# Kernel optimization log

Measured on AMD Instinct MI355X. Metric: run time of the kernel, lower is better.

## Reference

```python
import jax, jax.numpy as jnp
import numpy as np

D = 256          # embed_dim
NH = 4           # num_heads
NE = 16          # num_hyperedges
TC = 512         # text_channels
WIN = 64         # window size
EPS = 1e-5


def setup_inputs() -> dict:
    key = jax.random.key(0)
    ks = jax.random.split(key, 20)
    s = 0.02
    return {
        "feature_map": jax.random.normal(ks[0], (8, 256, 64, 64), jnp.float32),
        "text_features": jax.random.normal(ks[1], (8, 64, TC), jnp.float32),
        # qkv_gen: Conv2d(256->256,1x1), GELU, Conv2d(256->768,3x3,pad1), GroupNorm(4,768)
        "conv1_w": jax.random.normal(ks[2], (D, 256, 1, 1), jnp.float32) * s,
        "conv1_b": jnp.zeros((D,), jnp.float32),
        "conv2_w": jax.random.normal(ks[3], (3 * D, D, 3, 3), jnp.float32) * s,
        "conv2_b": jnp.zeros((3 * D,), jnp.float32),
        "gn_w": jnp.ones((3 * D,), jnp.float32),
        "gn_b": jnp.zeros((3 * D,), jnp.float32),
        # shared nn.MultiheadAttention params
        "in_proj_w": jax.random.normal(ks[4], (3 * D, D), jnp.float32) * s,
        "in_proj_b": jnp.zeros((3 * D,), jnp.float32),
        "out_proj_w": jax.random.normal(ks[5], (D, D), jnp.float32) * s,
        "out_proj_b": jnp.zeros((D,), jnp.float32),
        # text_adapter Linear(512->256)
        "txt_w": jax.random.normal(ks[6], (D, TC), jnp.float32) * s,
        "txt_b": jnp.zeros((D,), jnp.float32),
        # edge_predictor: Linear(512->256), GELU, Linear(256->16)
        "ep1_w": jax.random.normal(ks[7], (D, 2 * D), jnp.float32) * s,
        "ep1_b": jnp.zeros((D,), jnp.float32),
        "ep2_w": jax.random.normal(ks[8], (NE, D), jnp.float32) * s,
        "ep2_b": jnp.zeros((NE,), jnp.float32),
    }


def _gelu(x):
    return jax.nn.gelu(x, approximate=False)  # torch default is exact erf GELU


def _conv(x, w, b, pad):
    y = jax.lax.conv_general_dilated(x, w, (1, 1), [(pad, pad), (pad, pad)],
                                     dimension_numbers=("NCHW", "OIHW", "NCHW"))
    return y + b[None, :, None, None]


def _group_norm(x, w, b, groups=4):
    B, C, H, W = x.shape
    xg = x.reshape(B, groups, C // groups, H, W)
    mu = xg.mean(axis=(2, 3, 4), keepdims=True)
    var = xg.var(axis=(2, 3, 4), keepdims=True)
    xg = (xg - mu) * jax.lax.rsqrt(var + EPS)
    return xg.reshape(B, C, H, W) * w[None, :, None, None] + b[None, :, None, None]


def _mha(q, k, v, in_w, in_b, out_w, out_b):
    # torch nn.MultiheadAttention (batch_first), same-dim q/k/v
    Wq, Wk, Wv = in_w[:D], in_w[D:2 * D], in_w[2 * D:]
    bq, bk, bv = in_b[:D], in_b[D:2 * D], in_b[2 * D:]
    dh = D // NH

    def split(x, W, bias):
        y = x @ W.T + bias                      # [B,L,D]
        Bv, L, _ = y.shape
        return y.reshape(Bv, L, NH, dh).transpose(0, 2, 1, 3)  # [B,H,L,dh]

    qh, kh, vh = split(q, Wq, bq), split(k, Wk, bk), split(v, Wv, bv)
    scores = jnp.einsum("bhqd,bhkd->bhqk", qh, kh) / jnp.sqrt(jnp.float32(dh))
    attn = jax.nn.softmax(scores, axis=-1)
    o = jnp.einsum("bhqk,bhkd->bhqd", attn, vh)
    Bv, _, Lq, _ = o.shape
    o = o.transpose(0, 2, 1, 3).reshape(Bv, Lq, D)
    return o @ out_w.T + out_b


def reference(feature_map, text_features, conv1_w, conv1_b, conv2_w, conv2_b,
              gn_w, gn_b, in_proj_w, in_proj_b, out_proj_w, out_proj_b,
              txt_w, txt_b, ep1_w, ep1_b, ep2_w, ep2_b):
    B, C, H, W = feature_map.shape
    N = H * W
    # qkv_gen
    x = _gelu(_conv(feature_map, conv1_w, conv1_b, 0))
    qkv = _group_norm(_conv(x, conv2_w, conv2_b, 1), gn_w, gn_b)
    q, k, v = jnp.split(qkv, 3, axis=1)                    # each [B,D,H,W]
    to_seq = lambda t: t.reshape(B, D, N).transpose(0, 2, 1)  # [B,N,D]
    q_seq, k_seq, v_seq = to_seq(q), to_seq(k), to_seq(v)

    # text_adapter: Linear then AdaptiveAvgPool1d(4) over sequence (L=64 -> 4 bins of 16)
    t = text_features @ txt_w.T + txt_b                    # [B,L,D]
    L = t.shape[1]
    text_feat = t.reshape(B, 4, L // 4, D).mean(axis=2)    # [B,4,D]

    # hierarchical attention
    nw = N // WIN
    q_win = q_seq.reshape(B * nw, WIN, D)
    k_win = k_seq.reshape(B * nw, WIN, D)
    v_win = v_seq.reshape(B * nw, WIN, D)
    local = _mha(q_win, k_win, v_win, in_proj_w, in_proj_b, out_proj_w, out_proj_b)
    local = local.reshape(B, nw, WIN, D)
    global_q = local.mean(axis=2)                          # [B,nw,D]
    glob = _mha(global_q, text_feat, text_feat, in_proj_w, in_proj_b, out_proj_w, out_proj_b)
    glob = jnp.broadcast_to(glob[:, :, None, :], (B, nw, WIN, D))

    combined = jnp.concatenate([local.reshape(B, N, D), glob.reshape(B, N, D)], axis=-1)
    h = _gelu(combined @ ep1_w.T + ep1_b)
    return jax.nn.sigmoid(h @ ep2_w.T + ep2_b)             # [B,N,16]
```

## Files before the change

kernel.cpp:

```cpp
#include <hip/hip_runtime.h>

#define DEV __device__ __forceinline__

typedef __attribute__((ext_vector_type(8))) short bfx8;
typedef __attribute__((ext_vector_type(4))) float fx4;

typedef __attribute__((address_space(3))) unsigned int as3_u32;
typedef const __attribute__((address_space(1))) unsigned int as1_u32c;

DEV void gl_lds16(const void* g, const void* l) {
  __builtin_amdgcn_global_load_lds((as1_u32c*)(unsigned long long)g,
                                   (as3_u32*)(unsigned long long)l, 16, 0, 0);
}

DEV short f2bf(float f) {
  unsigned u = __float_as_uint(f);
  u += 0x7fffu + ((u >> 16) & 1u);
  return (short)(u >> 16);
}
DEV float bf2f(short s) {
  return __uint_as_float(((unsigned)(unsigned short)s) << 16);
}
DEV float gelu_f(float x) { return 0.5f * x * (1.0f + erff(x * 0.70710678118654752f)); }

#define MFMA16(acc, a, b) (acc) = __builtin_amdgcn_mfma_f32_16x16x32_bf16((a), (b), (acc), 0, 0, 0)

struct PrepArgs {
  const float *w1, *inw, *ow, *tw, *e1w, *e2w, *txt, *w2, *e1b, *ob, *tb, *inb;
  short *W1bf, *Wqkv, *Wo, *Wtxt, *Wep1, *Wep2, *W2t, *Wcomb;
  float *ebc, *khv, *vhv;
};

__global__ __launch_bounds__(256) void prep(PrepArgs a) {
  __shared__ char shmem[34816];
  const int bid = (int)blockIdx.x;
  const int t = threadIdx.x;
  if (bid < 290) {
    const float* src; short* dst; int st;
    if (bid < 32)       { src = a.w1;  dst = a.W1bf; st = 0; }
    else if (bid < 128) { src = a.inw; dst = a.Wqkv; st = 32; }
    else if (bid < 160) { src = a.ow;  dst = a.Wo;   st = 128; }
    else if (bid < 224) { src = a.tw;  dst = a.Wtxt; st = 160; }
    else if (bid < 288) { src = a.e1w; dst = a.Wep1; st = 224; }
    else                { src = a.e2w; dst = a.Wep2; st = 288; }
    long i = ((long)(bid - st) * 256 + t) * 8;
    bfx8 o;
    #pragma unroll
    for (int j = 0; j < 8; ++j) o[j] = f2bf(src[i + j]);
    *(bfx8*)(dst + i) = o;
  } else if (bid < 1058) {
    int oc = (bid - 290) * 256 + t;
    const float* s = a.w2 + (long)oc * 9;
    float v[9];
    #pragma unroll
    for (int j = 0; j < 9; ++j) v[j] = s[j];
    #pragma unroll
    for (int tap = 0; tap < 9; ++tap)
      a.W2t[(long)tap * (768 * 256) + oc] = f2bf(v[tap]);
  } else if (bid < 1122) {
    int n = (bid - 1058) * 4 + (t >> 6);
    int lane = t & 63;
    float s = 0.0f;
    #pragma unroll
    for (int i = 0; i < 4; ++i) {
      int c = lane + 64 * i;
      s += a.ob[c] * a.e1w[(long)n * 512 + c];
    }
    #pragma unroll
    for (int off = 1; off < 64; off <<= 1) s += __shfl_xor(s, off);
    if (lane == 0) a.ebc[n] = a.e1b[n] + s;
  } else if (bid < 1130) {
    float* tmean = (float*)shmem;
    float* tfb = (float*)(shmem + 8192);
    const int b = bid - 1122;
    {
      int key = t >> 6, d0 = (t & 63) * 8;
      float s[8] = {};
      const float* src = a.txt + ((long)(b * 64 + key * 16)) * 512 + d0;
      for (int i = 0; i < 16; ++i) {
        fx4 v0 = *(const fx4*)(src + (long)i * 512);
        fx4 v1 = *(const fx4*)(src + (long)i * 512 + 4);
        #pragma unroll
        for (int j = 0; j < 4; ++j) { s[j] += v0[j]; s[4 + j] += v1[j]; }
      }
      #pragma unroll
      for (int j = 0; j < 8; ++j) tmean[key * 512 + d0 + j] = s[j] * (1.0f / 16.0f);
    }
    __syncthreads();
    {
      int n = t;
      float a0 = 0, a1 = 0, a2 = 0, a3 = 0;
      const float* wr = a.tw + (long)n * 512;
      for (int d = 0; d < 512; d += 4) {
        fx4 w = *(const fx4*)(wr + d);
        #pragma unroll
        for (int j = 0; j < 4; ++j) {
          float wf = w[j];
          a0 += tmean[0 * 512 + d + j] * wf;
          a1 += tmean[1 * 512 + d + j] * wf;
          a2 += tmean[2 * 512 + d + j] * wf;
          a3 += tmean[3 * 512 + d + j] * wf;
        }
      }
      float bias = a.tb[n];
      tfb[0 * 256 + n] = a0 + bias; tfb[1 * 256 + n] = a1 + bias;
      tfb[2 * 256 + n] = a2 + bias; tfb[3 * 256 + n] = a3 + bias;
    }
    __syncthreads();
    {
      int n = t;
      const float* wk = a.inw + (long)(256 + n) * 256;
      const float* wvp = a.inw + (long)(512 + n) * 256;
      float k0=0,k1=0,k2=0,k3=0,v0=0,v1=0,v2=0,v3=0;
      for (int d = 0; d < 256; d += 4) {
        fx4 wkv = *(const fx4*)(wk + d);
        fx4 wvv = *(const fx4*)(wvp + d);
        #pragma unroll
        for (int j = 0; j < 4; ++j) {
          float f0 = tfb[0*256+d+j], f1 = tfb[1*256+d+j], f2 = tfb[2*256+d+j], f3 = tfb[3*256+d+j];
          float kw = wkv[j], vw = wvv[j];
          k0 += f0*kw; k1 += f1*kw; k2 += f2*kw; k3 += f3*kw;
          v0 += f0*vw; v1 += f1*vw; v2 += f2*vw; v3 += f3*vw;
        }
      }
      float bk = a.inb[256+n], bv = a.inb[512+n];
      a.khv[(b*4+0)*256+n]=k0+bk; a.khv[(b*4+1)*256+n]=k1+bk;
      a.khv[(b*4+2)*256+n]=k2+bk; a.khv[(b*4+3)*256+n]=k3+bk;
      a.vhv[(b*4+0)*256+n]=v0+bv; a.vhv[(b*4+1)*256+n]=v1+bv;
      a.vhv[(b*4+2)*256+n]=v2+bv; a.vhv[(b*4+3)*256+n]=v3+bv;
    }
  } else {
    short* Bt = (short*)shmem;
    const int idx = bid - 1130;
    const int bx = idx & 3, by = idx >> 2;
    const int lane = t & 63, w = t >> 6;
    const int lg = lane >> 4, li = lane & 15;
    const int m0 = by * 64, n0 = bx * 64;
    for (int id2 = t; id2 < 64 * 256; id2 += 256) {
      int c = id2 >> 6, d = id2 & 63;
      Bt[d * 264 + c] = f2bf(a.ow[(long)c * 256 + n0 + d]);
    }
    __syncthreads();
    fx4 acc[4] = {};
    const float* aR = a.e1w + (long)(m0 + w * 16 + li) * 512 + lg * 8;
    for (int kc = 0; kc < 256; kc += 32) {
      fx4 lo = *(const fx4*)(aR + kc);
      fx4 hi = *(const fx4*)(aR + kc + 4);
      bfx8 av;
      av[0] = f2bf(lo[0]); av[1] = f2bf(lo[1]); av[2] = f2bf(lo[2]); av[3] = f2bf(lo[3]);
      av[4] = f2bf(hi[0]); av[5] = f2bf(hi[1]); av[6] = f2bf(hi[2]); av[7] = f2bf(hi[3]);
      #pragma unroll
      for (int ni = 0; ni < 4; ++ni) {
        bfx8 bv = *(const bfx8*)(&Bt[(ni * 16 + li) * 264 + kc + lg * 8]);
        MFMA16(acc[ni], av, bv);
      }
    }
    #pragma unroll
    for (int ni = 0; ni < 4; ++ni)
      #pragma unroll
      for (int r = 0; r < 4; ++r)
        a.Wcomb[(long)(m0 + w * 16 + 4 * lg + r) * 256 + n0 + ni * 16 + li] = f2bf(acc[ni][r]);
  }
}

DEV int axc(int p, int c) { return p * 260 + (c ^ (((p >> 2) & 7) << 2)); }

__global__ __launch_bounds__(256) void tc1(const float* fm, const short* W1bf,
                                           const float* b1, short* xP) {
  __shared__ float Af[64 * 260];
  const int lane = threadIdx.x & 63, wv = threadIdx.x >> 6;
  const int lg = lane >> 4, li = lane & 15;
  const int y = blockIdx.x & 63, b = blockIdx.x >> 6;
  const int t = threadIdx.x;
  short* dstP = xP + ((long)b * 66 * 66 + (long)(y + 1) * 66 + 1) * 256;
  const bfx8 z8 = {0, 0, 0, 0, 0, 0, 0, 0};

  if (t < 64) {
    if (t < 32) *(bfx8*)(dstP - 256 + t * 8) = z8;
    else        *(bfx8*)(dstP + 64 * 256 + (t - 32) * 8) = z8;
  }
  if (y == 0) {
    short* top = xP + (long)b * 66 * 66 * 256;
    for (int i = t; i < 2112; i += 256) *(bfx8*)(top + i * 8) = z8;
  }
  if (y == 63) {
    short* bot = xP + ((long)b * 66 * 66 + 65 * 66) * 256;
    for (int i = t; i < 2112; i += 256) *(bfx8*)(bot + i * 8) = z8;
  }

  const float* src = fm + (long)b * 256 * 4096 + y * 64;
  #pragma unroll
  for (int i = 0; i < 16; ++i) {
    int chunk = i * 256 + t;
    int c = chunk >> 4;
    int q = chunk & 15;
    fx4 v = *(const fx4*)(src + (long)c * 4096 + q * 4);
    #pragma unroll
    for (int j = 0; j < 4; ++j) Af[axc(q * 4 + j, c)] = v[j];
  }
  __syncthreads();

  fx4 acc[4][4] = {};
  const short* Bb = W1bf + (long)(wv * 64 + li) * 256 + lg * 8;
  for (int c0 = 0; c0 < 256; c0 += 32) {
    bfx8 af[4], bfr[4];
    #pragma unroll
    for (int mi = 0; mi < 4; ++mi) {
      int p = mi * 16 + li;
      fx4 lo = *(const fx4*)(&Af[axc(p, c0 + lg * 8)]);
      fx4 hi = *(const fx4*)(&Af[axc(p, c0 + lg * 8 + 4)]);
      bfx8 tt;
      tt[0] = f2bf(lo[0]); tt[1] = f2bf(lo[1]); tt[2] = f2bf(lo[2]); tt[3] = f2bf(lo[3]);
      tt[4] = f2bf(hi[0]); tt[5] = f2bf(hi[1]); tt[6] = f2bf(hi[2]); tt[7] = f2bf(hi[3]);
      af[mi] = tt;
    }
    #pragma unroll
    for (int ni = 0; ni < 4; ++ni) bfr[ni] = *(const bfx8*)(Bb + ni * 16 * 256 + c0);
    #pragma unroll
    for (int mi = 0; mi < 4; ++mi)
      #pragma unroll
      for (int ni = 0; ni < 4; ++ni) MFMA16(acc[mi][ni], af[mi], bfr[ni]);
  }

  #pragma unroll
  for (int mi = 0; mi < 4; ++mi)
    #pragma unroll
    for (int ni = 0; ni < 4; ++ni) {
      int col = wv * 64 + ni * 16 + li;
      float bias = b1[col];
      #pragma unroll
      for (int r = 0; r < 4; ++r) {
        int x = mi * 16 + 4 * lg + r;
        dstP[(long)x * 256 + col] = f2bf(gelu_f(acc[mi][ni][r] + bias));
      }
    }
}

struct GemmP {
  const short* A; const short* B; void* O;
  const float* biasN; const float* biasM;
  long lda, ldb, ldo, sA, sB, sO;
  int M, N, K, outF32, act;
  int aShift;
  long sBN, sBM;
};

DEV void gemm_body64(const GemmP& g, int bx, int by, int bz) {
  __shared__ short As[2 * 128 * 32];
  __shared__ short Bs[2 * 128 * 32];
  const int lane = threadIdx.x & 63, wv = threadIdx.x >> 6;
  const int wm = wv >> 1, wn = wv & 1;
  const int lg = lane >> 4, li = lane & 15;
  const int m0 = by * 128, n0 = bx * 128, z = bz;
  const short* A = g.A + (long)z * g.sA + (long)(n0 >> 8) * g.aShift;
  const short* B = g.B + (long)z * g.sB;
  const int srow = wv * 16 + (lane >> 2);
  const int scol = (lane & 3) * 8;
  const short* pA0 = A + (long)(m0 + srow) * g.lda + scol;
  const short* pA1 = A + (long)(m0 + 64 + srow) * g.lda + scol;
  const short* pB0 = B + (long)(n0 + srow) * g.ldb + scol;
  const short* pB1 = B + (long)(n0 + 64 + srow) * g.ldb + scol;
  short* ldsA = As + wv * 512;
  short* ldsB = Bs + wv * 512;
  const short* aRd = As + (wm * 64 + li) * 32 + lg * 8;
  const short* bRd = Bs + (wn * 64 + li) * 32 + lg * 8;

  fx4 acc[4][4] = {};
  for (int kc = 0; kc < g.K; kc += 64) {
    gl_lds16(pA0 + kc, ldsA);
    gl_lds16(pA1 + kc, ldsA + 2048);
    gl_lds16(pA0 + kc + 32, ldsA + 4096);
    gl_lds16(pA1 + kc + 32, ldsA + 6144);
    gl_lds16(pB0 + kc, ldsB);
    gl_lds16(pB1 + kc, ldsB + 2048);
    gl_lds16(pB0 + kc + 32, ldsB + 4096);
    gl_lds16(pB1 + kc + 32, ldsB + 6144);
    __syncthreads();
    #pragma unroll
    for (int kk = 0; kk < 2; ++kk) {
      bfx8 af[4], bf[4];
      #pragma unroll
      for (int mi = 0; mi < 4; ++mi) af[mi] = *(const bfx8*)(aRd + kk * 4096 + mi * 16 * 32);
      #pragma unroll
      for (int ni = 0; ni < 4; ++ni) bf[ni] = *(const bfx8*)(bRd + kk * 4096 + ni * 16 * 32);
      #pragma unroll
      for (int mi = 0; mi < 4; ++mi)
        #pragma unroll
        for (int ni = 0; ni < 4; ++ni)
          MFMA16(acc[mi][ni], af[mi], bf[ni]);
    }
    __syncthreads();
  }

  #pragma unroll
  for (int mi = 0; mi < 4; ++mi)
    #pragma unroll
    for (int ni = 0; ni < 4; ++ni) {
      int col = n0 + wn * 64 + ni * 16 + li;
      int rowb = m0 + wm * 64 + mi * 16 + 4 * lg;
      float bn = g.biasN ? g.biasN[(long)z * g.sBN + col] : 0.0f;
      #pragma unroll
      for (int r = 0; r < 4; ++r) {
        int row = rowb + r;
        float v = acc[mi][ni][r] + bn;
        if (g.biasM) v += g.biasM[(long)z * g.sBM + row];
        if (g.act == 1) v = gelu_f(v);
        long oidx = (long)z * g.sO + (long)row * g.ldo + col;
        if (g.outF32) ((float*)g.O)[oidx] = v;
        else ((short*)g.O)[oidx] = f2bf(v);
      }
    }
}

__global__ __launch_bounds__(256) void projk(GemmP gq, GemmP gv) {
  int bid = (int)blockIdx.x;
  int id = (bid & 7) * 192 + (bid >> 3);
  if (id < 1024) {
    int z = id >> 7, r = id & 127;
    gemm_body64(gq, r & 3, r >> 2, z);
  } else {
    int j = id - 1024;
    int z = j >> 6, r = j & 63;
    gemm_body64(gv, r & 31, r >> 5, z);
  }
}

__global__ __launch_bounds__(256) void conv2g(const short* xP, const short* W2t,
                                              const float* b2, short* qkv, float* stats) {
  __shared__ short As[2 * 128 * 32];
  __shared__ short Bs[2 * 128 * 32];
  __shared__ float red[4][4];
  const int lane = threadIdx.x & 63, wv = threadIdx.x >> 6;
  const int wm = wv >> 1, wn = wv & 1;
  const int lg = lane >> 4, li = lane & 15;
  const int w = ((int)blockIdx.x & 7) * 192 + ((int)blockIdx.x >> 3);
  const int n0 = (w % 6) * 128;
  const int by = w / 6;
  const int b = by >> 5, ypair = by & 31;
  const short* xPb = xP + (long)b * 66 * 66 * 256;

  const int srow = wv * 16 + (lane >> 2);
  const int scol = (lane & 3) * 8;
  long baseA[2], baseB[2];
  #pragma unroll
  for (int j = 0; j < 2; ++j) {
    int r = j * 64 + srow;
    int yy = 2 * ypair + (r >> 6);
    int x = r & 63;
    baseA[j] = ((long)yy * 66 + x) * 256 + scol;
    baseB[j] = (long)(n0 + r) * 256 + scol;
  }
  short* ldsA = As + wv * 512;
  short* ldsB = Bs + wv * 512;
  const short* aRd = As + (wm * 64 + li) * 32 + lg * 8;
  const short* bRd = Bs + (wn * 64 + li) * 32 + lg * 8;

  fx4 acc[4][4] = {};
  for (int ks = 0; ks < 36; ++ks) {
    int tap = ks >> 2;
    int c0 = (ks & 3) * 64;
    int dy = tap / 3, dx = tap - dy * 3;
    long aoff = (long)(dy * 66 + dx) * 256 + c0;
    long boff = (long)tap * (768 * 256) + c0;
    gl_lds16(xPb + baseA[0] + aoff, ldsA);
    gl_lds16(xPb + baseA[1] + aoff, ldsA + 2048);
    gl_lds16(xPb + baseA[0] + aoff + 32, ldsA + 4096);
    gl_lds16(xPb + baseA[1] + aoff + 32, ldsA + 6144);
    gl_lds16(W2t + baseB[0] + boff, ldsB);
    gl_lds16(W2t + baseB[1] + boff, ldsB + 2048);
    gl_lds16(W2t + baseB[0] + boff + 32, ldsB + 4096);
    gl_lds16(W2t + baseB[1] + boff + 32, ldsB + 6144);
    __syncthreads();
    #pragma unroll
    for (int kk = 0; kk < 2; ++kk) {
      bfx8 af[4], bf[4];
      #pragma unroll
      for (int mi = 0; mi < 4; ++mi) af[mi] = *(const bfx8*)(aRd + kk * 4096 + mi * 16 * 32);
      #pragma unroll
      for (int ni = 0; ni < 4; ++ni) bf[ni] = *(const bfx8*)(bRd + kk * 4096 + ni * 16 * 32);
      #pragma unroll
      for (int mi = 0; mi < 4; ++mi)
        #pragma unroll
        for (int ni = 0; ni < 4; ++ni)
          MFMA16(acc[mi][ni], af[mi], bf[ni]);
    }
    __syncthreads();
  }

  const int g0 = n0 / 192;
  const int bnd = (g0 + 1) * 192;
  float sA = 0.0f, s2A = 0.0f, sB = 0.0f, s2B = 0.0f;
  const long prow0 = (long)b * 4096 + (long)ypair * 128 + wm * 64 + 4 * lg;
  #pragma unroll
  for (int ni = 0; ni < 4; ++ni) {
    int col = n0 + wn * 64 + ni * 16 + li;
    float bias = b2[col];
    bool inA = (col < bnd);
    #pragma unroll
    for (int mi = 0; mi < 4; ++mi) {
      long rb = prow0 + mi * 16;
      #pragma unroll
      for (int r = 0; r < 4; ++r) {
        float v = acc[mi][ni][r] + bias;
        if (inA) { sA += v; s2A += v * v; } else { sB += v; s2B += v * v; }
        qkv[(rb + r) * 768 + col] = f2bf(v);
      }
    }
  }
  #pragma unroll
  for (int off = 1; off < 64; off <<= 1) {
    sA += __shfl_xor(sA, off);  s2A += __shfl_xor(s2A, off);
    sB += __shfl_xor(sB, off);  s2B += __shfl_xor(s2B, off);
  }
  if (lane == 0) { red[wv][0] = sA; red[wv][1] = s2A; red[wv][2] = sB; red[wv][3] = s2B; }
  __syncthreads();
  if (threadIdx.x == 0) {
    float a1 = red[0][0] + red[1][0] + red[2][0] + red[3][0];
    float a2 = red[0][1] + red[1][1] + red[2][1] + red[3][1];
    atomicAdd(&stats[(b * 4 + g0) * 2], a1);
    atomicAdd(&stats[(b * 4 + g0) * 2 + 1], a2);
    if (bnd < n0 + 128) {
      float b1s = red[0][2] + red[1][2] + red[2][2] + red[3][2];
      float b2s = red[0][3] + red[1][3] + red[2][3] + red[3][3];
      atomicAdd(&stats[(b * 4 + g0 + 1) * 2], b1s);
      atomicAdd(&stats[(b * 4 + g0 + 1) * 2 + 1], b2s);
    }
  }
}

__global__ __launch_bounds__(256) void gn_fold(const float* stats, const float* gnw, const float* gnb,
                                               const float* inw, const float* inb,
                                               short* Wf, float* bfold) {
  const int lane = threadIdx.x & 63, wv = threadIdx.x >> 6;
  const int row = blockIdx.x * 4 + wv;
  const int b = row / 768, j = row - b * 768;
  const int cb = (j >> 8) << 8;
  const float nrm = 1.0f / (192.0f * 4096.0f);
  float part = 0.0f;
  #pragma unroll
  for (int i = 0; i < 4; ++i) {
    int c = lane + 64 * i;
    int cg = cb + c;
    int grp = cg / 192;
    float s1 = stats[(b * 4 + grp) * 2];
    float s2 = stats[(b * 4 + grp) * 2 + 1];
    float mu = s1 * nrm;
    float var = s2 * nrm - mu * mu;
    float rs = rsqrtf(var + 1e-5f);
    float s = rs * gnw[cg];
    float t = gnb[cg] - mu * s;
    float wv_ = inw[(long)j * 256 + c];
    Wf[(long)row * 256 + c] = f2bf(wv_ * s);
    part += t * wv_;
  }
  #pragma unroll
  for (int off = 1; off < 64; off <<= 1) part += __shfl_xor(part, off);
  if (lane == 0) bfold[row] = inb[j] + part;
}

__global__ __launch_bounds__(256) void attn_local(const short* qk, const short* vhT,
                                                  short* oat, short* oatm) {
  __shared__ short Pl[4 * 64 * 72];
  const int lane = threadIdx.x & 63, h = threadIdx.x >> 6;
  const int lg = lane >> 4, li = lane & 15;
  const int bw = blockIdx.x;
  const int b = bw >> 6, wY = bw & 63;
  const long p0 = (long)bw * 64;

  bfx8 qf[4][2], kf[4][2];
  #pragma unroll
  for (int mi = 0; mi < 4; ++mi)
    #pragma unroll
    for (int ks = 0; ks < 2; ++ks) {
      qf[mi][ks] = *(const bfx8*)(qk + (p0 + 16 * mi + li) * 512 + h * 64 + 32 * ks + 8 * lg);
      kf[mi][ks] = *(const bfx8*)(qk + (p0 + 16 * mi + li) * 512 + 256 + h * 64 + 32 * ks + 8 * lg);
    }
  fx4 s[4][4] = {};
  #pragma unroll
  for (int mi = 0; mi < 4; ++mi)
    #pragma unroll
    for (int ni = 0; ni < 4; ++ni) {
      MFMA16(s[mi][ni], qf[mi][0], kf[ni][0]);
      MFMA16(s[mi][ni], qf[mi][1], kf[ni][1]);
    }
  #pragma unroll
  for (int mi = 0; mi < 4; ++mi)
    #pragma unroll
    for (int ni = 0; ni < 4; ++ni) s[mi][ni] *= 0.125f;

  #pragma unroll
  for (int mi = 0; mi < 4; ++mi)
    #pragma unroll
    for (int r = 0; r < 4; ++r) {
      float mx = fmaxf(fmaxf(s[mi][0][r], s[mi][1][r]), fmaxf(s[mi][2][r], s[mi][3][r]));
      for (int off = 1; off < 16; off <<= 1) mx = fmaxf(mx, __shfl_xor(mx, off));
      float e[4];
      float sum = 0.0f;
      #pragma unroll
      for (int ni = 0; ni < 4; ++ni) { e[ni] = expf(s[mi][ni][r] - mx); sum += e[ni]; }
      for (int off = 1; off < 16; off <<= 1) sum += __shfl_xor(sum, off);
      float inv = 1.0f / sum;
      int row = h * 64 + 16 * mi + 4 * lg + r;
      #pragma unroll
      for (int ni = 0; ni < 4; ++ni) Pl[row * 72 + 16 * ni + li] = f2bf(e[ni] * inv);
    }
  __syncthreads();

  fx4 o[4][4] = {};
  #pragma unroll
  for (int ks = 0; ks < 2; ++ks) {
    bfx8 pf[4], vf[4];
    #pragma unroll
    for (int mi = 0; mi < 4; ++mi)
      pf[mi] = *(const bfx8*)(&Pl[(h * 64 + 16 * mi + li) * 72 + 32 * ks + 8 * lg]);
    #pragma unroll
    for (int ni = 0; ni < 4; ++ni)
      vf[ni] = *(const bfx8*)(vhT + ((long)(b * 256 + h * 64 + 16 * ni + li)) * 4096 + wY * 64 + 32 * ks + 8 * lg);
    #pragma unroll
    for (int mi = 0; mi < 4; ++mi)
      #pragma unroll
      for (int ni = 0; ni < 4; ++ni) MFMA16(o[mi][ni], pf[mi], vf[ni]);
  }
  #pragma unroll
  for (int mi = 0; mi < 4; ++mi)
    #pragma unroll
    for (int ni = 0; ni < 4; ++ni)
      #pragma unroll
      for (int r = 0; r < 4; ++r)
        oat[(p0 + 16 * mi + 4 * lg + r) * 256 + h * 64 + 16 * ni + li] = f2bf(o[mi][ni][r]);

  #pragma unroll
  for (int ni = 0; ni < 4; ++ni) {
    float s2 = 0.0f;
    #pragma unroll
    for (int mi = 0; mi < 4; ++mi)
      #pragma unroll
      for (int r = 0; r < 4; ++r) s2 += o[mi][ni][r];
    s2 += __shfl_xor(s2, 16);
    s2 += __shfl_xor(s2, 32);
    if (lg == 0)
      oatm[(long)bw * 256 + h * 64 + 16 * ni + li] = f2bf(s2 * (1.0f / 64.0f));
  }
}

#define GP 272

DEV void mm_stage(const short* srcA, const short* Bw, long ldb, const float* biasN,
                  short* dstL, float* dstG, int wv, int lg, int li) {
  fx4 acc[4][4] = {};
  const short* aRd = srcA + li * GP + lg * 8;
  const short* bR = Bw + (long)(wv * 64 + li) * ldb + lg * 8;
  for (int kc = 0; kc < 256; kc += 32) {
    bfx8 af[4], bf[4];
    #pragma unroll
    for (int mi = 0; mi < 4; ++mi) af[mi] = *(const bfx8*)(aRd + mi * 16 * GP + kc);
    #pragma unroll
    for (int ni = 0; ni < 4; ++ni) bf[ni] = *(const bfx8*)(bR + (long)ni * 16 * ldb + kc);
    #pragma unroll
    for (int mi = 0; mi < 4; ++mi)
      #pragma unroll
      for (int ni = 0; ni < 4; ++ni) MFMA16(acc[mi][ni], af[mi], bf[ni]);
  }
  #pragma unroll
  for (int mi = 0; mi < 4; ++mi)
    #pragma unroll
    for (int ni = 0; ni < 4; ++ni) {
      int col = wv * 64 + ni * 16 + li;
      float bn = biasN[col];
      #pragma unroll
      for (int r = 0; r < 4; ++r) {
        int row = mi * 16 + 4 * lg + r;
        float v = acc[mi][ni][r] + bn;
        if (dstL) dstL[row * GP + col] = f2bf(v);
        else dstG[(long)row * 256 + col] = v;
      }
    }
}

__global__ __launch_bounds__(256) void globk2(
    const short* oatm, const float* khv, const float* vhv,
    const short* Wo, const short* Wqkv, const short* Wep1,
    const float* ob, const float* inb, const float* ebc,
    float* gcon) {
  __shared__ short bufA[64 * GP];
  __shared__ short bufB[64 * GP];
  __shared__ float kh_s[4][256];
  __shared__ float vh_s[4][256];
  const int t = threadIdx.x;
  const int lane = t & 63, wv = t >> 6;
  const int lg = lane >> 4, li = lane & 15;
  const int b = blockIdx.x;

  {
    #pragma unroll
    for (int i = 0; i < 8; ++i) {
      int chunk = i * 256 + t;
      int row = chunk >> 5, colc = (chunk & 31) * 8;
      *(bfx8*)(bufA + row * GP + colc) =
          *(const bfx8*)(oatm + ((long)(b * 64 + row)) * 256 + colc);
    }
    #pragma unroll
    for (int key = 0; key < 4; ++key) {
      kh_s[key][t] = khv[(long)(b * 4 + key) * 256 + t];
      vh_s[key][t] = vhv[(long)(b * 4 + key) * 256 + t];
    }
  }
  __syncthreads();
  mm_stage(bufA, Wo, 256, ob, bufB, nullptr, wv, lg, li);
  __syncthreads();
  mm_stage(bufB, Wqkv, 256, inb, bufA, nullptr, wv, lg, li);
  __syncthreads();
  {
    int p = t >> 2, h = t & 3;
    const short* qr = bufA + p * GP + h * 64;
    float sc[4];
    #pragma unroll
    for (int key = 0; key < 4; ++key) {
      float s = 0.0f;
      for (int d = 0; d < 64; d += 8) {
        bfx8 q8 = *(const bfx8*)(qr + d);
        #pragma unroll
        for (int j = 0; j < 8; ++j) s += bf2f(q8[j]) * kh_s[key][h * 64 + d + j];
      }
      sc[key] = s * 0.125f;
    }
    float mx = fmaxf(fmaxf(sc[0], sc[1]), fmaxf(sc[2], sc[3]));
    float e0 = expf(sc[0]-mx), e1 = expf(sc[1]-mx), e2 = expf(sc[2]-mx), e3 = expf(sc[3]-mx);
    float inv = 1.0f / (e0 + e1 + e2 + e3);
    e0 *= inv; e1 *= inv; e2 *= inv; e3 *= inv;
    short* orow = bufB + p * GP + h * 64;
    for (int d = 0; d < 64; ++d) {
      float o = e0*vh_s[0][h*64+d] + e1*vh_s[1][h*64+d] + e2*vh_s[2][h*64+d] + e3*vh_s[3][h*64+d];
      orow[d] = f2bf(o);
    }
  }
  __syncthreads();
  mm_stage(bufB, Wo, 256, ob, bufA, nullptr, wv, lg, li);
  __syncthreads();
  mm_stage(bufA, Wep1 + 256, 512, ebc, nullptr, gcon + (long)b * 64 * 256, wv, lg, li);
}

__global__ __launch_bounds__(256) void ep12(const short* oat, const short* Wcomb,
                                            const short* Wep2, const float* gcon,
                                            const float* e2b, float* out) {
  __shared__ short As[2 * 128 * 32];
  __shared__ short Bs[2 * 128 * 32];
  __shared__ short hl[128 * 140];
  const int lane = threadIdx.x & 63, wv = threadIdx.x >> 6;
  const int wm = wv >> 1, wn = wv & 1;
  const int lg = lane >> 4, li = lane & 15;
  const int m0 = (int)blockIdx.x * 128;
  const int srow = wv * 16 + (lane >> 2);
  const int scol = (lane & 3) * 8;
  const short* pA0 = oat + (long)(m0 + srow) * 256 + scol;
  const short* pA1 = oat + (long)(m0 + 64 + srow) * 256 + scol;
  short* ldsA = As + wv * 512;
  short* ldsB = Bs + wv * 512;
  const short* aRd = As + (wm * 64 + li) * 32 + lg * 8;
  const short* bRd = Bs + (wn * 64 + li) * 32 + lg * 8;

  fx4 eacc[2] = {};
  for (int half = 0; half < 2; ++half) {
    const short* B = Wcomb + (long)(half * 128) * 256;
    const short* pB0 = B + (long)srow * 256 + scol;
    const short* pB1 = B + (long)(64 + srow) * 256 + scol;
    fx4 acc[4][4] = {};
    for (int kc = 0; kc < 256; kc += 64) {
      gl_lds16(pA0 + kc, ldsA);
      gl_lds16(pA1 + kc, ldsA + 2048);
      gl_lds16(pA0 + kc + 32, ldsA + 4096);
      gl_lds16(pA1 + kc + 32, ldsA + 6144);
      gl_lds16(pB0 + kc, ldsB);
      gl_lds16(pB1 + kc, ldsB + 2048);
      gl_lds16(pB0 + kc + 32, ldsB + 4096);
      gl_lds16(pB1 + kc + 32, ldsB + 6144);
      __syncthreads();
      #pragma unroll
      for (int kk = 0; kk < 2; ++kk) {
        bfx8 af[4], bf[4];
        #pragma unroll
        for (int mi = 0; mi < 4; ++mi) af[mi] = *(const bfx8*)(aRd + kk * 4096 + mi * 16 * 32);
        #pragma unroll
        for (int ni = 0; ni < 4; ++ni) bf[ni] = *(const bfx8*)(bRd + kk * 4096 + ni * 16 * 32);
        #pragma unroll
        for (int mi = 0; mi < 4; ++mi)
          #pragma unroll
          for (int ni = 0; ni < 4; ++ni)
            MFMA16(acc[mi][ni], af[mi], bf[ni]);
      }
      __syncthreads();
    }
    #pragma unroll
    for (int mi = 0; mi < 4; ++mi)
      #pragma unroll
      for (int ni = 0; ni < 4; ++ni) {
        int coll = wn * 64 + ni * 16 + li;
        int colg = half * 128 + coll;
        #pragma unroll
        for (int r = 0; r < 4; ++r) {
          int rowl = wm * 64 + mi * 16 + 4 * lg + r;
          float v = acc[mi][ni][r] + gcon[(long)((m0 + rowl) >> 6) * 256 + colg];
          hl[rowl * 140 + coll] = f2bf(gelu_f(v));
        }
      }
    __syncthreads();
    #pragma unroll
    for (int kc = 0; kc < 128; kc += 32) {
      bfx8 bf2v = *(const bfx8*)(Wep2 + (long)li * 256 + half * 128 + kc + lg * 8);
      #pragma unroll
      for (int mi = 0; mi < 2; ++mi) {
        bfx8 af = *(const bfx8*)(hl + (wv * 32 + mi * 16 + li) * 140 + kc + lg * 8);
        MFMA16(eacc[mi], af, bf2v);
      }
    }
    __syncthreads();
  }
  #pragma unroll
  for (int mi = 0; mi < 2; ++mi)
    #pragma unroll
    for (int r = 0; r < 4; ++r) {
      int row = m0 + wv * 32 + mi * 16 + 4 * lg + r;
      out[(long)row * 16 + li] = 1.0f / (1.0f + expf(-(eacc[mi][r] + e2b[li])));
    }
}

extern "C" void kernel_launch(void* const* d_in, const int* in_sizes, int n_in,
                              void* d_out, int out_size, void* d_ws, size_t ws_size,
                              hipStream_t stream) {
  (void)in_sizes; (void)n_in; (void)out_size; (void)ws_size;
  const float* fm  = (const float*)d_in[0];
  const float* txt = (const float*)d_in[1];
  const float* w1  = (const float*)d_in[2];
  const float* b1  = (const float*)d_in[3];
  const float* w2  = (const float*)d_in[4];
  const float* b2  = (const float*)d_in[5];
  const float* gnw = (const float*)d_in[6];
  const float* gnb = (const float*)d_in[7];
  const float* inw = (const float*)d_in[8];
  const float* inb = (const float*)d_in[9];
  const float* ow  = (const float*)d_in[10];
  const float* ob  = (const float*)d_in[11];
  const float* tw  = (const float*)d_in[12];
  const float* tb  = (const float*)d_in[13];
  const float* e1w = (const float*)d_in[14];
  const float* e1b = (const float*)d_in[15];
  const float* e2w = (const float*)d_in[16];
  const float* e2b = (const float*)d_in[17];
  float* out = (float*)d_out;

  char* base = (char*)d_ws;
  size_t off = 0;
  auto alloc = [&](size_t bytes) -> char* {
    char* r = base + off;
    off = (off + bytes + 255) & ~(size_t)255;
    return r;
  };
  short* W1bf = (short*)alloc(256 * 256 * 2);
  short* W2t  = (short*)alloc((size_t)9 * 768 * 256 * 2);
  short* Wqkv = (short*)alloc(768 * 256 * 2);
  short* Wo   = (short*)alloc(256 * 256 * 2);
  short* Wcomb= (short*)alloc(256 * 256 * 2);
  float* ebc  = (float*)alloc(256 * 4);
  short* Wtxt = (short*)alloc(256 * 512 * 2);
  short* Wep1 = (short*)alloc(256 * 512 * 2);
  short* Wep2 = (short*)alloc(16 * 256 * 2);
  short* xP   = (short*)alloc((size_t)8 * 66 * 66 * 256 * 2);
  short* qkv  = (short*)alloc((size_t)8 * 4096 * 768 * 2);
  float* stats= (float*)alloc(64 * 4);
  short* Wf   = (short*)alloc((size_t)8 * 768 * 256 * 2);
  float* bfold= (float*)alloc((size_t)8 * 768 * 4);
  short* qk   = (short*)alloc((size_t)32768 * 512 * 2);
  short* vhT  = (short*)alloc((size_t)8 * 4096 * 256 * 2);
  short* oat  = (short*)alloc((size_t)8 * 4096 * 256 * 2);
  short* oatm = (short*)alloc(512 * 256 * 2);
  float* khv  = (float*)alloc(8 * 4 * 256 * 4);
  float* vhv  = (float*)alloc(8 * 4 * 256 * 4);
  float* gcon = (float*)alloc(512 * 256 * 4);

  hipMemsetAsync(stats, 0, 64 * 4, stream);

  PrepArgs pa;
  pa.w1 = w1; pa.inw = inw; pa.ow = ow; pa.tw = tw; pa.e1w = e1w; pa.e2w = e2w;
  pa.txt = txt; pa.w2 = w2; pa.e1b = e1b; pa.ob = ob; pa.tb = tb; pa.inb = inb;
  pa.W1bf = W1bf; pa.Wqkv = Wqkv; pa.Wo = Wo; pa.Wtxt = Wtxt; pa.Wep1 = Wep1;
  pa.Wep2 = Wep2; pa.W2t = W2t; pa.Wcomb = Wcomb;
  pa.ebc = ebc; pa.khv = khv; pa.vhv = vhv;
  prep<<<1146, 256, 0, stream>>>(pa);

  tc1<<<512, 256, 0, stream>>>(fm, W1bf, b1, xP);

  conv2g<<<1536, 256, 0, stream>>>(xP, W2t, b2, qkv, stats);

  gn_fold<<<1536, 256, 0, stream>>>(stats, gnw, gnb, inw, inb, Wf, bfold);

  {
    GemmP gq{};
    gq.A = qkv; gq.lda = 768; gq.sA = 4096L * 768;
    gq.B = Wf; gq.ldb = 256; gq.sB = 768L * 256;
    gq.O = qk; gq.ldo = 512; gq.sO = 4096L * 512;
    gq.biasN = bfold; gq.sBN = 768;
    gq.aShift = 256;
    gq.M = 4096; gq.N = 512; gq.K = 256;
    GemmP gv{};
    gv.A = Wf + 512 * 256; gv.lda = 256; gv.sA = 768L * 256;
    gv.B = qkv + 512; gv.ldb = 768; gv.sB = 4096L * 768;
    gv.O = vhT; gv.ldo = 4096; gv.sO = 256L * 4096;
    gv.biasM = bfold + 512; gv.sBM = 768;
    gv.M = 256; gv.N = 4096; gv.K = 256;
    projk<<<1536, 256, 0, stream>>>(gq, gv);
  }

  attn_local<<<512, 256, 0, stream>>>(qk, vhT, oat, oatm);

  globk2<<<8, 256, 0, stream>>>(oatm, khv, vhv, Wo, Wqkv, Wep1, ob, inb, ebc, gcon);

  ep12<<<256, 256, 0, stream>>>(oat, Wcomb, Wep2, gcon, e2b, out);
}
```

Measured before the change: 325.1 us.

## Fuse global attention path into edge-predictor kernel, recomputing per block

Removes the separate 8-block globk2 kernel. Each of the 256 ep12 blocks now recomputes the whole per-batch global chain (out-proj, in-proj, 4-key attention, out-proj, ep1 half) for 64 windows and keeps only the two rows it needs in LDS, sharing memory with the GEMM buffers through a union. This drops a serialized, low-occupancy launch and the gcon round trip through global memory, at the cost of 32x redundant small GEMM work per batch. Block indices in attn_local and ep12 are also swizzled so that consecutive blocks land on different batches.

Result: faster. 317.9 us (-2.2%).

```diff
diff --git a/kernel.cpp b/kernel.cpp
--- a/kernel.cpp
+++ b/kernel.cpp
@@ -463,7 +463,7 @@
   __shared__ short Pl[4 * 64 * 72];
   const int lane = threadIdx.x & 63, h = threadIdx.x >> 6;
   const int lg = lane >> 4, li = lane & 15;
-  const int bw = blockIdx.x;
+  const int bw = (((int)blockIdx.x & 7) << 6) | ((int)blockIdx.x >> 3);
   const int b = bw >> 6, wY = bw & 63;
   const long p0 = (long)bw * 64;
 
@@ -546,7 +546,7 @@
 #define GP 272
 
 DEV void mm_stage(const short* srcA, const short* Bw, long ldb, const float* biasN,
-                  short* dstL, float* dstG, int wv, int lg, int li) {
+                  short* dstL, int wv, int lg, int li) {
   fx4 acc[4][4] = {};
   const short* aRd = srcA + li * GP + lg * 8;
   const short* bR = Bw + (long)(wv * 64 + li) * ldb + lg * 8;
@@ -570,49 +570,55 @@
       #pragma unroll
       for (int r = 0; r < 4; ++r) {
         int row = mi * 16 + 4 * lg + r;
-        float v = acc[mi][ni][r] + bn;
-        if (dstL) dstL[row * GP + col] = f2bf(v);
-        else dstG[(long)row * 256 + col] = v;
-      }
-    }
-}
-
-__global__ __launch_bounds__(256) void globk2(
-    const short* oatm, const float* khv, const float* vhv,
-    const short* Wo, const short* Wqkv, const short* Wep1,
-    const float* ob, const float* inb, const float* ebc,
-    float* gcon) {
-  __shared__ short bufA[64 * GP];
-  __shared__ short bufB[64 * GP];
-  __shared__ float kh_s[4][256];
-  __shared__ float vh_s[4][256];
+        dstL[row * GP + col] = f2bf(acc[mi][ni][r] + bn);
+      }
+    }
+}
+
+union EpU {
+  struct { short bufA[64 * GP]; short bufB[64 * GP]; float kh[4][256]; float vh[4][256]; } c;
+  struct { short As[2 * 128 * 32]; short Bs[2 * 128 * 32]; short hl[128 * 140]; } m;
+};
+
+__global__ __launch_bounds__(256) void ep12(const short* oat, const short* oatm,
+                                            const float* khv, const float* vhv,
+                                            const short* Wo, const short* Wqkv, const short* Wep1,
+                                            const short* Wcomb, const short* Wep2,
+                                            const float* ob, const float* inb, const float* ebc,
+                                            const float* e2b, float* out) {
+  __shared__ EpU u;
+  __shared__ float gcon_s[2][256];
   const int t = threadIdx.x;
   const int lane = t & 63, wv = t >> 6;
+  const int wm = wv >> 1, wn = wv & 1;
   const int lg = lane >> 4, li = lane & 15;
-  const int b = blockIdx.x;
+  const int mb = (((int)blockIdx.x & 7) << 5) | ((int)blockIdx.x >> 3);
+  const int m0 = mb * 128;
+  const int b = m0 >> 12;
+  const int ib = mb & 31;
 
   {
     #pragma unroll
     for (int i = 0; i < 8; ++i) {
       int chunk = i * 256 + t;
       int row = chunk >> 5, colc = (chunk & 31) * 8;
-      *(bfx8*)(bufA + row * GP + colc) =
+      *(bfx8*)(u.c.bufA + row * GP + colc) =
           *(const bfx8*)(oatm + ((long)(b * 64 + row)) * 256 + colc);
     }
     #pragma unroll
     for (int key = 0; key < 4; ++key) {
-      kh_s[key][t] = khv[(long)(b * 4 + key) * 256 + t];
-      vh_s[key][t] = vhv[(long)(b * 4 + key) * 256 + t];
+      u.c.kh[key][t] = khv[(long)(b * 4 + key) * 256 + t];
+      u.c.vh[key][t] = vhv[(long)(b * 4 + key) * 256 + t];
     }
   }
   __syncthreads();
-  mm_stage(bufA, Wo, 256, ob, bufB, nullptr, wv, lg, li);
+  mm_stage(u.c.bufA, Wo, 256, ob, u.c.bufB, wv, lg, li);
   __syncthreads();
-  mm_stage(bufB, Wqkv, 256, inb, bufA, nullptr, wv, lg, li);
+  mm_stage(u.c.bufB, Wqkv, 256, inb, u.c.bufA, wv, lg, li);
   __syncthreads();
   {
-    int p = t >> 2, h = t & 3;
-    const short* qr = bufA + p * GP + h * 64;
+    int p = t >> 2, hh = t & 3;
+    const short* qr = u.c.bufA + p * GP + hh * 64;
     float sc[4];
     #pragma unroll
     for (int key = 0; key < 4; ++key) {
@@ -620,7 +626,7 @@
       for (int d = 0; d < 64; d += 8) {
         bfx8 q8 = *(const bfx8*)(qr + d);
         #pragma unroll
-        for (int j = 0; j < 8; ++j) s += bf2f(q8[j]) * kh_s[key][h * 64 + d + j];
+        for (int j = 0; j < 8; ++j) s += bf2f(q8[j]) * u.c.kh[key][hh * 64 + d + j];
       }
       sc[key] = s * 0.125f;
     }
@@ -628,36 +634,54 @@
     float e0 = expf(sc[0]-mx), e1 = expf(sc[1]-mx), e2 = expf(sc[2]-mx), e3 = expf(sc[3]-mx);
     float inv = 1.0f / (e0 + e1 + e2 + e3);
     e0 *= inv; e1 *= inv; e2 *= inv; e3 *= inv;
-    short* orow = bufB + p * GP + h * 64;
+    short* orow = u.c.bufB + p * GP + hh * 64;
     for (int d = 0; d < 64; ++d) {
-      float o = e0*vh_s[0][h*64+d] + e1*vh_s[1][h*64+d] + e2*vh_s[2][h*64+d] + e3*vh_s[3][h*64+d];
+      float o = e0*u.c.vh[0][hh*64+d] + e1*u.c.vh[1][hh*64+d] +
+                e2*u.c.vh[2][hh*64+d] + e3*u.c.vh[3][hh*64+d];
       orow[d] = f2bf(o);
     }
   }
   __syncthreads();
-  mm_stage(bufB, Wo, 256, ob, bufA, nullptr, wv, lg, li);
+  mm_stage(u.c.bufB, Wo, 256, ob, u.c.bufA, wv, lg, li);
   __syncthreads();
-  mm_stage(bufA, Wep1 + 256, 512, ebc, nullptr, gcon + (long)b * 64 * 256, wv, lg, li);
-}
-
-__global__ __launch_bounds__(256) void ep12(const short* oat, const short* Wcomb,
-                                            const short* Wep2, const float* gcon,
-                                            const float* e2b, float* out) {
-  __shared__ short As[2 * 128 * 32];
-  __shared__ short Bs[2 * 128 * 32];
-  __shared__ short hl[128 * 140];
-  const int lane = threadIdx.x & 63, wv = threadIdx.x >> 6;
-  const int wm = wv >> 1, wn = wv & 1;
-  const int lg = lane >> 4, li = lane & 15;
-  const int m0 = (int)blockIdx.x * 128;
+  {
+    fx4 acc[4][4] = {};
+    const short* aRd = u.c.bufA + li * GP + lg * 8;
+    const short* bR = Wep1 + 256 + (long)(wv * 64 + li) * 512 + lg * 8;
+    for (int kc = 0; kc < 256; kc += 32) {
+      bfx8 af[4], bf[4];
+      #pragma unroll
+      for (int mi = 0; mi < 4; ++mi) af[mi] = *(const bfx8*)(aRd + mi * 16 * GP + kc);
+      #pragma unroll
+      for (int ni = 0; ni < 4; ++ni) bf[ni] = *(const bfx8*)(bR + (long)ni * 16 * 512 + kc);
+      #pragma unroll
+      for (int mi = 0; mi < 4; ++mi)
+        #pragma unroll
+        for (int ni = 0; ni < 4; ++ni) MFMA16(acc[mi][ni], af[mi], bf[ni]);
+    }
+    #pragma unroll
+    for (int mi = 0; mi < 4; ++mi)
+      #pragma unroll
+      for (int ni = 0; ni < 4; ++ni) {
+        int col = wv * 64 + ni * 16 + li;
+        float bn = ebc[col];
+        #pragma unroll
+        for (int r = 0; r < 4; ++r) {
+          int row = mi * 16 + 4 * lg + r;
+          if ((row >> 1) == ib) gcon_s[row & 1][col] = acc[mi][ni][r] + bn;
+        }
+      }
+  }
+  __syncthreads();
+
   const int srow = wv * 16 + (lane >> 2);
   const int scol = (lane & 3) * 8;
   const short* pA0 = oat + (long)(m0 + srow) * 256 + scol;
   const short* pA1 = oat + (long)(m0 + 64 + srow) * 256 + scol;
-  short* ldsA = As + wv * 512;
-  short* ldsB = Bs + wv * 512;
-  const short* aRd = As + (wm * 64 + li) * 32 + lg * 8;
-  const short* bRd = Bs + (wn * 64 + li) * 32 + lg * 8;
+  short* ldsA = u.m.As + wv * 512;
+  short* ldsB = u.m.Bs + wv * 512;
+  const short* aRd = u.m.As + (wm * 64 + li) * 32 + lg * 8;
+  const short* bRd = u.m.Bs + (wn * 64 + li) * 32 + lg * 8;
 
   fx4 eacc[2] = {};
   for (int half = 0; half < 2; ++half) {
@@ -699,8 +723,8 @@
         #pragma unroll
         for (int r = 0; r < 4; ++r) {
           int rowl = wm * 64 + mi * 16 + 4 * lg + r;
-          float v = acc[mi][ni][r] + gcon[(long)((m0 + rowl) >> 6) * 256 + colg];
-          hl[rowl * 140 + coll] = f2bf(gelu_f(v));
+          float v = acc[mi][ni][r] + gcon_s[rowl >> 6][colg];
+          u.m.hl[rowl * 140 + coll] = f2bf(gelu_f(v));
         }
       }
     __syncthreads();
@@ -709,7 +733,7 @@
       bfx8 bf2v = *(const bfx8*)(Wep2 + (long)li * 256 + half * 128 + kc + lg * 8);
       #pragma unroll
       for (int mi = 0; mi < 2; ++mi) {
-        bfx8 af = *(const bfx8*)(hl + (wv * 32 + mi * 16 + li) * 140 + kc + lg * 8);
+        bfx8 af = *(const bfx8*)(u.m.hl + (wv * 32 + mi * 16 + li) * 140 + kc + lg * 8);
         MFMA16(eacc[mi], af, bf2v);
       }
     }
@@ -775,7 +799,6 @@
   short* oatm = (short*)alloc(512 * 256 * 2);
   float* khv  = (float*)alloc(8 * 4 * 256 * 4);
   float* vhv  = (float*)alloc(8 * 4 * 256 * 4);
-  float* gcon = (float*)alloc(512 * 256 * 4);
 
   hipMemsetAsync(stats, 0, 64 * 4, stream);
 
@@ -812,7 +835,6 @@
 
   attn_local<<<512, 256, 0, stream>>>(qk, vhT, oat, oatm);
 
-  globk2<<<8, 256, 0, stream>>>(oatm, khv, vhv, Wo, Wqkv, Wep1, ob, inb, ebc, gcon);
-
-  ep12<<<256, 256, 0, stream>>>(oat, Wcomb, Wep2, gcon, e2b, out);
-}
+  ep12<<<256, 256, 0, stream>>>(oat, oatm, khv, vhv, Wo, Wqkv, Wep1, Wcomb, Wep2,
+                                ob, inb, ebc, e2b, out);
+}
```
